# Performance work log

Measured on AMD Instinct MI355X. Metric: run time of the kernel, lower is better.

The kernel has to match this reference:

```python
import jax, jax.numpy as jnp
import numpy as np

L, NH, DH, D, DI, V = 12, 12, 64, 768, 3072, 10000
QLEN, MLEN, CLEN, BSZ = 512, 512, 32, 4
EPS = 1e-5


def _ln(x, g, b):
    m = x.mean(-1, keepdims=True)
    v = ((x - m) ** 2).mean(-1, keepdims=True)
    return (x - m) / jnp.sqrt(v + EPS) * g + b


def _rel_shift(x):
    # x: [B, H, qlen, rlen]; Transformer-XL pad/reshape shift trick
    B, H, q, r = x.shape
    xp = jnp.pad(x, ((0, 0), (0, 0), (0, 0), (1, 0)))
    return xp.reshape(B, H, r + 1, q)[:, :, 1:, :].reshape(B, H, q, r)


def _pos_emb(klen):
    # positions klen-1 .. 0 (relative distances), sinusoidal, dim D
    pos = jnp.arange(klen - 1, -1, -1, dtype=jnp.float32)
    inv = 1.0 / (10000.0 ** (jnp.arange(0, D, 2, dtype=jnp.float32) / D))
    s = pos[:, None] * inv[None, :]
    return jnp.concatenate([jnp.sin(s), jnp.cos(s)], axis=-1)  # [klen, D]


def setup_inputs() -> dict:
    key = jax.random.key(0)
    ks = jax.random.split(key, 21)
    init = lambda k, shape: (0.02 * jax.random.normal(k, shape)).astype(jnp.float32)
    return {
        'x': jax.random.randint(ks[0], (QLEN, BSZ), 0, V),
        'condition': init(ks[1], (CLEN, BSZ, D)) * 50.0,
        'mems': init(ks[2], (L, MLEN, BSZ, D)) * 50.0,
        'emb': init(ks[3], (V, D)),
        'qkv_w': init(ks[4], (L, D, 3 * NH * DH)),
        'r_net_w': init(ks[5], (L, D, NH * DH)),
        'o_w': init(ks[6], (L, NH * DH, D)),
        'ln1_g': jnp.ones((L, D), jnp.float32),
        'ln1_b': jnp.zeros((L, D), jnp.float32),
        'w1': init(ks[7], (L, D, DI)),
        'b1': jnp.zeros((L, DI), jnp.float32),
        'w2': init(ks[8], (L, DI, D)),
        'b2': jnp.zeros((L, D), jnp.float32),
        'ln2_g': jnp.ones((L, D), jnp.float32),
        'ln2_b': jnp.zeros((L, D), jnp.float32),
        'r_w_bias': init(ks[9], (NH, DH)),
        'r_r_bias': init(ks[10], (NH, DH)),
        'proj_w': init(ks[11], (D, V)),
        'proj_b': jnp.zeros((V,), jnp.float32),
    }


def reference(x, condition, mems, emb, qkv_w, r_net_w, o_w, ln1_g, ln1_b,
              w1, b1, w2, b2, ln2_g, ln2_b, r_w_bias, r_r_bias, proj_w, proj_b):
    qlen, bsz = x.shape
    klen = CLEN + MLEN + qlen
    h = emb[x] * jnp.sqrt(jnp.float32(D))  # [qlen, B, D] word emb * sqrt(d_model)
    r = _pos_emb(klen)                      # [klen, D]
    scale = 1.0 / jnp.sqrt(jnp.float32(DH))
    # causal mask: query i may attend to keys j <= CLEN + MLEN + i (True = masked)
    mask = jnp.arange(klen)[None, :] > (jnp.arange(qlen)[:, None] + CLEN + MLEN)
    for l in range(L):
        cat = jnp.concatenate([condition, mems[l], h], axis=0)  # [klen, B, D]
        heads = cat @ qkv_w[l]                                   # [klen, B, 3*NH*DH]
        qh, kh, vh = jnp.split(heads, 3, axis=-1)
        qh = qh[-qlen:].reshape(qlen, bsz, NH, DH)
        kh = kh.reshape(klen, bsz, NH, DH)
        vh = vh.reshape(klen, bsz, NH, DH)
        rk = (r @ r_net_w[l]).reshape(klen, NH, DH)
        AC = jnp.einsum('ibnd,jbnd->bnij', qh + r_w_bias, kh)    # content score
        BD = _rel_shift(jnp.einsum('ibnd,jnd->bnij', qh + r_r_bias, rk))  # position score
        score = (AC + BD) * scale
        score = jnp.where(mask[None, None], -jnp.inf, score)
        prob = jax.nn.softmax(score, axis=-1)
        av = jnp.einsum('bnij,jbnd->ibnd', prob, vh).reshape(qlen, bsz, NH * DH)
        h = _ln(h + av @ o_w[l], ln1_g[l], ln1_b[l])             # post-LN attention
        ff = jax.nn.relu(h @ w1[l] + b1[l]) @ w2[l] + b2[l]
        h = _ln(h + ff, ln2_g[l], ln2_b[l])                      # post-LN FFN
    return h @ proj_w + proj_b  # [qlen, B, n_token] logits
```

## Files before the change

### kernel.cpp

```cpp
#include <hip/hip_runtime.h>
#include <stdint.h>

#define NLAYER 12
#define NH 12
#define DH 64
#define DMODEL 768
#define DI 3072
#define NV 10000
#define QLEN 512
#define MLEN 512
#define CLEN 32
#define BSZ 4
#define KLEN (CLEN + MLEN + QLEN)
#define MQ (QLEN * BSZ)
#define MK (KLEN * BSZ)
#define H3 (3 * NH * DH)
#define HD (NH * DH)
#define NG (BSZ * NH)
#define SROW ((size_t)QLEN * KLEN)
#define KPAD_R 1152
#define NPAD_V 10112

typedef __bf16 bf16;
typedef __bf16 bf16x8 __attribute__((ext_vector_type(8)));
typedef float f32x4 __attribute__((ext_vector_type(4)));

__device__ __forceinline__ void gload16(const void* g, void* l) {
    __builtin_amdgcn_global_load_lds((const __attribute__((address_space(1))) void*)g,
                                     (__attribute__((address_space(3))) void*)l, 16, 0, 0);
}

__device__ __forceinline__ void split_store(float x, bf16* __restrict__ hp,
                                            bf16* __restrict__ lp, size_t off) {
    bf16 h = (bf16)x;
    hp[off] = h;
    lp[off] = (bf16)(x - (float)h);
}

__device__ __forceinline__ void raster(int& bx, int& by) {
    int gx = gridDim.x, gy = gridDim.y;
    int nwg = gx * gy;
    int wgid = blockIdx.y * gx + blockIdx.x;
    int q = nwg >> 3, r = nwg & 7;
    int xcd = wgid & 7, lin = wgid >> 3;
    int swz = (xcd < r ? xcd * (q + 1) : r * (q + 1) + (xcd - r) * q) + lin;
    int gsz = gx * 4;
    int grp = swz / gsz, rem = swz % gsz;
    int rows = gy - grp * 4;
    if (rows > 4) rows = 4;
    bx = rem / rows;
    by = grp * 4 + rem % rows;
}

__global__ __launch_bounds__(256) void k_embed(const int* __restrict__ x,
                                               const float* __restrict__ emb,
                                               float* __restrict__ h) {
    int idx = blockIdx.x * 256 + threadIdx.x;
    if (idx >= MQ * DMODEL) return;
    int row = idx / DMODEL;
    int d = idx % DMODEL;
    int tok = x[row];
    h[idx] = emb[(size_t)tok * DMODEL + d] * 27.712812921102035f;
}

__global__ __launch_bounds__(256) void k_posemb(bf16* __restrict__ rh, bf16* __restrict__ rl) {
    int idx = blockIdx.x * 256 + threadIdx.x;
    if (idx >= KPAD_R * DMODEL) return;
    int k = idx / DMODEL;
    int d = idx % DMODEL;
    float v = 0.0f;
    if (k < KLEN) {
        int pos = KLEN - 1 - k;
        int j = (d < DMODEL / 2) ? d : d - DMODEL / 2;
        double inv = exp(-((double)(2 * j) / (double)DMODEL) * log(10000.0));
        double s = (double)pos * inv;
        v = (d < DMODEL / 2) ? (float)sin(s) : (float)cos(s);
    }
    split_store(v, rh, rl, (size_t)idx);
}

__global__ __launch_bounds__(256) void k_concat(const float* __restrict__ cond,
                                                const float* __restrict__ mem_l,
                                                const float* __restrict__ h,
                                                bf16* __restrict__ catH,
                                                bf16* __restrict__ catL) {
    int idx = blockIdx.x * 256 + threadIdx.x;
    if (idx >= MK * DMODEL) return;
    int row = idx / DMODEL;
    int k = row / BSZ;
    float v;
    if (k < CLEN) v = cond[idx];
    else if (k < CLEN + MLEN) v = mem_l[idx - CLEN * BSZ * DMODEL];
    else v = h[idx - (CLEN + MLEN) * BSZ * DMODEL];
    split_store(v, catH, catL, (size_t)idx);
}

__global__ __launch_bounds__(256) void k_wconv(const float* __restrict__ W,
                                               bf16* __restrict__ Bh,
                                               bf16* __restrict__ Bl,
                                               int K, int N) {
    __shared__ float t[32][33];
    int n0 = blockIdx.x * 32, k0 = blockIdx.y * 32;
    int tc = threadIdx.x & 31, tr = threadIdx.x >> 5;
#pragma unroll
    for (int i = 0; i < 32; i += 8) {
        int n = n0 + tc;
        t[tr + i][tc] = (n < N) ? W[(size_t)(k0 + tr + i) * N + n] : 0.0f;
    }
    __syncthreads();
#pragma unroll
    for (int i = 0; i < 32; i += 8) {
        int n = n0 + tr + i;
        int k = k0 + tc;
        float x = t[tc][tr + i];
        size_t off = (size_t)n * K + k;
        bf16 h = (bf16)x;
        Bh[off] = h;
        Bl[off] = (bf16)(x - (float)h);
    }
}

template <int BM, bool BIAS, bool RELU, bool SPLITOUT>
__global__ __launch_bounds__(256) void k_mgemm(const bf16* __restrict__ Ahi,
                                               const bf16* __restrict__ Alo,
                                               const bf16* __restrict__ Bhi,
                                               const bf16* __restrict__ Blo,
                                               const float* __restrict__ bias,
                                               float* __restrict__ C,
                                               bf16* __restrict__ Chi,
                                               bf16* __restrict__ Clo,
                                               int M, int N, int K, int ldc) {
    constexpr int MI = (BM == 128) ? 4 : 2;
    __shared__ __align__(16) bf16 As[2][BM][32];
    __shared__ __align__(16) bf16 Bs[2][128][32];
    int bx, by;
    raster(bx, by);
    int tid = threadIdx.x;
    int lane = tid & 63;
    int wave = tid >> 6;
    int bm = by * BM, bn = bx * 128;
    int wr = (wave >> 1) * (BM / 2), wc = (wave & 1) * 64;
    int fr = lane & 15;
    int fk = (lane >> 4) * 8;

    const f32x4 fzero = {0.f, 0.f, 0.f, 0.f};
    f32x4 acc[MI][4];
#pragma unroll
    for (int i = 0; i < MI; i++)
#pragma unroll
        for (int j = 0; j < 4; j++) acc[i][j] = fzero;

    int r0 = tid >> 2, p0 = (tid & 3) * 8;
    int r1 = r0 + 64, p1 = p0;

    for (int k0 = 0; k0 < K; k0 += 32) {
        if (BM == 128) {
            gload16(Ahi + (size_t)(bm + r0) * K + k0 + p0, &As[0][r0][p0]);
            gload16(Ahi + (size_t)(bm + r1) * K + k0 + p1, &As[0][r1 & (BM - 1)][p1]);
            gload16(Alo + (size_t)(bm + r0) * K + k0 + p0, &As[1][r0][p0]);
            gload16(Alo + (size_t)(bm + r1) * K + k0 + p1, &As[1][r1 & (BM - 1)][p1]);
        } else {
            gload16(Ahi + (size_t)(bm + r0) * K + k0 + p0, &As[0][r0 & (BM - 1)][p0]);
            gload16(Alo + (size_t)(bm + r0) * K + k0 + p0, &As[1][r0 & (BM - 1)][p0]);
        }
        gload16(Bhi + (size_t)(bn + r0) * K + k0 + p0, &Bs[0][r0][p0]);
        gload16(Bhi + (size_t)(bn + r1) * K + k0 + p1, &Bs[0][r1][p1]);
        gload16(Blo + (size_t)(bn + r0) * K + k0 + p0, &Bs[1][r0][p0]);
        gload16(Blo + (size_t)(bn + r1) * K + k0 + p1, &Bs[1][r1][p1]);
        __syncthreads();

        bf16x8 ah[MI], al[MI], bh[4], bl[4];
#pragma unroll
        for (int mi = 0; mi < MI; mi++) {
            ah[mi] = *(const bf16x8*)&As[0][wr + mi * 16 + fr][fk];
            al[mi] = *(const bf16x8*)&As[1][wr + mi * 16 + fr][fk];
        }
#pragma unroll
        for (int ni = 0; ni < 4; ni++) {
            bh[ni] = *(const bf16x8*)&Bs[0][wc + ni * 16 + fr][fk];
            bl[ni] = *(const bf16x8*)&Bs[1][wc + ni * 16 + fr][fk];
        }
#pragma unroll
        for (int mi = 0; mi < MI; mi++)
#pragma unroll
            for (int ni = 0; ni < 4; ni++) {
                acc[mi][ni] = __builtin_amdgcn_mfma_f32_16x16x32_bf16(ah[mi], bh[ni], acc[mi][ni], 0, 0, 0);
                acc[mi][ni] = __builtin_amdgcn_mfma_f32_16x16x32_bf16(ah[mi], bl[ni], acc[mi][ni], 0, 0, 0);
                acc[mi][ni] = __builtin_amdgcn_mfma_f32_16x16x32_bf16(al[mi], bh[ni], acc[mi][ni], 0, 0, 0);
            }
        __syncthreads();
    }

#pragma unroll
    for (int mi = 0; mi < MI; mi++) {
        int rowb = bm + wr + mi * 16 + (lane >> 4) * 4;
#pragma unroll
        for (int ni = 0; ni < 4; ni++) {
            int col = bn + wc + ni * 16 + fr;
            if (col >= N) continue;
            float bv = BIAS ? bias[col] : 0.0f;
#pragma unroll
            for (int r = 0; r < 4; r++) {
                int row = rowb + r;
                if (row >= M) continue;
                float xv = acc[mi][ni][r] + bv;
                if (RELU) xv = fmaxf(xv, 0.0f);
                size_t off = (size_t)row * ldc + col;
                if (SPLITOUT) {
                    bf16 hh = (bf16)xv;
                    Chi[off] = hh;
                    Clo[off] = (bf16)(xv - (float)hh);
                } else {
                    C[off] = xv;
                }
            }
        }
    }
}

__global__ __launch_bounds__(256) void k_qprep(const float* __restrict__ heads,
                                               const float* __restrict__ rwb,
                                               const float* __restrict__ rrb,
                                               bf16* __restrict__ qwH, bf16* __restrict__ qwL,
                                               bf16* __restrict__ qrH, bf16* __restrict__ qrL) {
    int idx = blockIdx.x * 256 + threadIdx.x;
    if (idx >= NG * QLEN * DH) return;
    int g = idx >> 15;
    int rem = idx & 32767;
    int i = rem >> 6;
    int d = rem & 63;
    int b = g / NH, n = g % NH;
    float q = heads[((size_t)((CLEN + MLEN + i) * BSZ + b)) * H3 + n * DH + d];
    split_store(q + rwb[n * DH + d], qwH, qwL, (size_t)idx);
    split_store(q + rrb[n * DH + d], qrH, qrL, (size_t)idx);
}

__global__ __launch_bounds__(256) void k_kconv(const float* __restrict__ heads,
                                               bf16* __restrict__ khH, bf16* __restrict__ khL,
                                               int g0, int ngc) {
    int idx = blockIdx.x * 256 + threadIdx.x;
    if (idx >= ngc * KPAD_R * DH) return;
    int gl = idx / (KPAD_R * DH);
    int rem = idx % (KPAD_R * DH);
    int j = rem >> 6, d = rem & 63;
    int g = g0 + gl, b = g / NH, n = g % NH;
    float v = (j < KLEN) ? heads[(size_t)(j * BSZ + b) * H3 + HD + n * DH + d] : 0.0f;
    split_store(v, khH, khL, (size_t)idx);
}

__global__ __launch_bounds__(256) void k_vtconv(const float* __restrict__ heads,
                                                bf16* __restrict__ vtH, bf16* __restrict__ vtL,
                                                int g0) {
    __shared__ float t[32][33];
    int gl = blockIdx.z;
    int g = g0 + gl, b = g / NH, n = g % NH;
    int j0 = blockIdx.x * 32, d0 = blockIdx.y * 32;
    int tc = threadIdx.x & 31, tr = threadIdx.x >> 5;
#pragma unroll
    for (int i = 0; i < 32; i += 8)
        t[tr + i][tc] = heads[(size_t)((j0 + tr + i) * BSZ + b) * H3 + 2 * HD + n * DH + d0 + tc];
    __syncthreads();
#pragma unroll
    for (int i = 0; i < 32; i += 8)
        split_store(t[tc][tr + i], vtH, vtL,
                    ((size_t)gl * DH + d0 + tr + i) * KLEN + j0 + tc);
}

template <bool SHIFT>
__global__ __launch_bounds__(256) void k_score(const bf16* __restrict__ QH,
                                               const bf16* __restrict__ QL,
                                               const bf16* __restrict__ KHp,
                                               const bf16* __restrict__ KLp,
                                               float* __restrict__ sAc,
                                               int g0) {
    int gl = blockIdx.z;
    int g = g0 + gl;
    int n = g % NH;
    const bf16* Ah = QH + (size_t)g * QLEN * DH;
    const bf16* Al = QL + (size_t)g * QLEN * DH;
    const bf16 *Bh, *Bl;
    int ldb;
    if (SHIFT) { Bh = KHp + n * DH; Bl = KLp + n * DH; ldb = HD; }
    else { Bh = KHp + (size_t)gl * KPAD_R * DH; Bl = KLp + (size_t)gl * KPAD_R * DH; ldb = DH; }
    float* C = sAc + (size_t)gl * SROW;

    __shared__ __align__(16) bf16 As[2][128][32];
    __shared__ __align__(16) bf16 Bs[2][128][32];
    int tid = threadIdx.x;
    int lane = tid & 63;
    int wave = tid >> 6;
    int bm = blockIdx.y * 128, bn = blockIdx.x * 128;
    int wr = (wave >> 1) * 64, wc = (wave & 1) * 64;
    int fr = lane & 15;
    int fk = (lane >> 4) * 8;

    const f32x4 fzero = {0.f, 0.f, 0.f, 0.f};
    f32x4 acc[4][4];
#pragma unroll
    for (int i = 0; i < 4; i++)
#pragma unroll
        for (int j = 0; j < 4; j++) acc[i][j] = fzero;

    int r0 = tid >> 2, p0 = (tid & 3) * 8;
    int r1 = r0 + 64, p1 = p0;

#pragma unroll
    for (int k0 = 0; k0 < DH; k0 += 32) {
        gload16(Ah + (size_t)(bm + r0) * DH + k0 + p0, &As[0][r0][p0]);
        gload16(Ah + (size_t)(bm + r1) * DH + k0 + p1, &As[0][r1][p1]);
        gload16(Al + (size_t)(bm + r0) * DH + k0 + p0, &As[1][r0][p0]);
        gload16(Al + (size_t)(bm + r1) * DH + k0 + p1, &As[1][r1][p1]);
        gload16(Bh + (size_t)(bn + r0) * ldb + k0 + p0, &Bs[0][r0][p0]);
        gload16(Bh + (size_t)(bn + r1) * ldb + k0 + p1, &Bs[0][r1][p1]);
        gload16(Bl + (size_t)(bn + r0) * ldb + k0 + p0, &Bs[1][r0][p0]);
        gload16(Bl + (size_t)(bn + r1) * ldb + k0 + p1, &Bs[1][r1][p1]);
        __syncthreads();

        bf16x8 ah[4], al[4], bh[4], bl[4];
#pragma unroll
        for (int mi = 0; mi < 4; mi++) {
            ah[mi] = *(const bf16x8*)&As[0][wr + mi * 16 + fr][fk];
            al[mi] = *(const bf16x8*)&As[1][wr + mi * 16 + fr][fk];
        }
#pragma unroll
        for (int ni = 0; ni < 4; ni++) {
            bh[ni] = *(const bf16x8*)&Bs[0][wc + ni * 16 + fr][fk];
            bl[ni] = *(const bf16x8*)&Bs[1][wc + ni * 16 + fr][fk];
        }
#pragma unroll
        for (int mi = 0; mi < 4; mi++)
#pragma unroll
            for (int ni = 0; ni < 4; ni++) {
                acc[mi][ni] = __builtin_amdgcn_mfma_f32_16x16x32_bf16(ah[mi], bh[ni], acc[mi][ni], 0, 0, 0);
                acc[mi][ni] = __builtin_amdgcn_mfma_f32_16x16x32_bf16(ah[mi], bl[ni], acc[mi][ni], 0, 0, 0);
                acc[mi][ni] = __builtin_amdgcn_mfma_f32_16x16x32_bf16(al[mi], bh[ni], acc[mi][ni], 0, 0, 0);
            }
        __syncthreads();
    }

#pragma unroll
    for (int mi = 0; mi < 4; mi++) {
        int rowb = bm + wr + mi * 16 + (lane >> 4) * 4;
#pragma unroll
        for (int ni = 0; ni < 4; ni++) {
            int t = bn + wc + ni * 16 + fr;
            if (t >= KLEN) continue;
#pragma unroll
            for (int r = 0; r < 4; r++) {
                int i = rowb + r;
                if (SHIFT) {
                    int j = t - (QLEN - 1) + i;
                    if (j >= 0) C[(size_t)i * KLEN + j] += acc[mi][ni][r];
                } else {
                    C[(size_t)i * KLEN + t] = acc[mi][ni][r];
                }
            }
        }
    }
}

__global__ __launch_bounds__(256) void k_softmax_p(const float* __restrict__ sAc,
                                                   bf16* __restrict__ P) {
    __shared__ float red[256];
    int i = blockIdx.x;
    int gl = blockIdx.y;
    int tid = threadIdx.x;
    const float* row = sAc + (size_t)gl * SROW + (size_t)i * KLEN;
    bf16* pr = P + (size_t)gl * SROW + (size_t)i * KLEN;
    int len = i + CLEN + MLEN + 1;
    float v[5];
    int cnt = 0;
    float mx = -1e30f;
    for (int j = tid; j < len; j += 256) {
        float s = row[j] * 0.125f;
        v[cnt++] = s;
        mx = fmaxf(mx, s);
    }
    red[tid] = mx;
    __syncthreads();
    for (int st = 128; st > 0; st >>= 1) {
        if (tid < st) red[tid] = fmaxf(red[tid], red[tid + st]);
        __syncthreads();
    }
    float smax = red[0];
    __syncthreads();
    float sum = 0.f;
    cnt = 0;
    for (int j = tid; j < len; j += 256) {
        float e = __expf(v[cnt] - smax);
        v[cnt] = e;
        sum += e;
        cnt++;
    }
    red[tid] = sum;
    __syncthreads();
    for (int st = 128; st > 0; st >>= 1) {
        if (tid < st) red[tid] += red[tid + st];
        __syncthreads();
    }
    float inv = 1.0f / red[0];
    cnt = 0;
    for (int j = tid; j < len; j += 256) pr[j] = (bf16)(v[cnt++] * inv);
    for (int j = tid; j < KLEN; j += 256)
        if (j >= len) pr[j] = (bf16)0.0f;
}

__global__ __launch_bounds__(256) void k_av(const bf16* __restrict__ P,
                                            const bf16* __restrict__ VH,
                                            const bf16* __restrict__ VL,
                                            bf16* __restrict__ atH,
                                            bf16* __restrict__ atL,
                                            int g0) {
    int gl = blockIdx.z;
    int g = g0 + gl;
    int b = g / NH, n = g % NH;
    const bf16* Ap = P + (size_t)gl * SROW;
    const bf16* Vh = VH + (size_t)gl * DH * KLEN;
    const bf16* Vl = VL + (size_t)gl * DH * KLEN;
    __shared__ __align__(16) bf16 As[64][32];
    __shared__ __align__(16) bf16 Bs[2][64][32];
    int tid = threadIdx.x;
    int lane = tid & 63;
    int wave = tid >> 6;
    int bm = blockIdx.y * 64;
    int fr = lane & 15;
    int fk = (lane >> 4) * 8;
    const f32x4 fzero = {0.f, 0.f, 0.f, 0.f};
    f32x4 acc[4] = {fzero, fzero, fzero, fzero};
    int ra = tid >> 2, pa = (tid & 3) * 8;

    for (int k0 = 0; k0 < KLEN; k0 += 32) {
        gload16(Ap + (size_t)(bm + ra) * KLEN + k0 + pa, &As[ra][pa]);
        gload16(Vh + (size_t)ra * KLEN + k0 + pa, &Bs[0][ra][pa]);
        gload16(Vl + (size_t)ra * KLEN + k0 + pa, &Bs[1][ra][pa]);
        __syncthreads();
        bf16x8 a = *(const bf16x8*)&As[wave * 16 + fr][fk];
#pragma unroll
        for (int ni = 0; ni < 4; ni++) {
            bf16x8 bh = *(const bf16x8*)&Bs[0][ni * 16 + fr][fk];
            bf16x8 bl = *(const bf16x8*)&Bs[1][ni * 16 + fr][fk];
            acc[ni] = __builtin_amdgcn_mfma_f32_16x16x32_bf16(a, bh, acc[ni], 0, 0, 0);
            acc[ni] = __builtin_amdgcn_mfma_f32_16x16x32_bf16(a, bl, acc[ni], 0, 0, 0);
        }
        __syncthreads();
    }

#pragma unroll
    for (int ni = 0; ni < 4; ni++) {
        int d = ni * 16 + fr;
#pragma unroll
        for (int r = 0; r < 4; r++) {
            int i = bm + wave * 16 + (lane >> 4) * 4 + r;
            size_t off = (size_t)(i * BSZ + b) * HD + n * DH + d;
            split_store(acc[ni][r], atH, atL, off);
        }
    }
}

__global__ __launch_bounds__(256) void k_add_ln(float* __restrict__ h,
                                                const float* __restrict__ delta,
                                                const float* __restrict__ g,
                                                const float* __restrict__ bta,
                                                bf16* __restrict__ hH,
                                                bf16* __restrict__ hL) {
    __shared__ float xs[DMODEL];
    __shared__ float red[256];
    int row = blockIdx.x;
    int tid = threadIdx.x;
    float* hr = h + (size_t)row * DMODEL;
    const float* dr = delta + (size_t)row * DMODEL;
    float s = 0.f;
    for (int d = tid; d < DMODEL; d += 256) {
        float v = hr[d] + dr[d];
        xs[d] = v;
        s += v;
    }
    red[tid] = s;
    __syncthreads();
    for (int st = 128; st > 0; st >>= 1) {
        if (tid < st) red[tid] += red[tid + st];
        __syncthreads();
    }
    float mean = red[0] * (1.0f / DMODEL);
    __syncthreads();
    float v2 = 0.f;
    for (int d = tid; d < DMODEL; d += 256) {
        float t = xs[d] - mean;
        v2 += t * t;
    }
    red[tid] = v2;
    __syncthreads();
    for (int st = 128; st > 0; st >>= 1) {
        if (tid < st) red[tid] += red[tid + st];
        __syncthreads();
    }
    float inv = rsqrtf(red[0] * (1.0f / DMODEL) + 1e-5f);
    for (int d = tid; d < DMODEL; d += 256) {
        float y = (xs[d] - mean) * inv * g[d] + bta[d];
        hr[d] = y;
        split_store(y, hH, hL, (size_t)row * DMODEL + d);
    }
}

extern "C" void kernel_launch(void* const* d_in, const int* in_sizes, int n_in,
                              void* d_out, int out_size, void* d_ws, size_t ws_size,
                              hipStream_t stream) {
    const int* x = (const int*)d_in[0];
    const float* condition = (const float*)d_in[1];
    const float* mems = (const float*)d_in[2];
    const float* emb = (const float*)d_in[3];
    const float* qkv_w = (const float*)d_in[4];
    const float* r_net_w = (const float*)d_in[5];
    const float* o_w = (const float*)d_in[6];
    const float* ln1_g = (const float*)d_in[7];
    const float* ln1_b = (const float*)d_in[8];
    const float* w1 = (const float*)d_in[9];
    const float* b1 = (const float*)d_in[10];
    const float* w2 = (const float*)d_in[11];
    const float* b2 = (const float*)d_in[12];
    const float* ln2_g = (const float*)d_in[13];
    const float* ln2_b = (const float*)d_in[14];
    const float* r_w_bias = (const float*)d_in[15];
    const float* r_r_bias = (const float*)d_in[16];
    const float* proj_w = (const float*)d_in[17];
    const float* proj_b = (const float*)d_in[18];
    float* out = (float*)d_out;

    float* ws = (float*)d_ws;
    float* h = ws;
    float* heads = h + (size_t)MQ * DMODEL;
    float* delta = heads + (size_t)MK * H3;

    bf16* pb = (bf16*)(delta + (size_t)MQ * DMODEL);
    bf16* rbH = pb; pb += (size_t)KPAD_R * DMODEL;
    bf16* rbL = pb; pb += (size_t)KPAD_R * DMODEL;
    bf16* atH = pb; pb += (size_t)MQ * HD;
    bf16* atL = pb; pb += (size_t)MQ * HD;
    bf16* qwH = pb; pb += (size_t)NG * QLEN * DH;
    bf16* qwL = pb; pb += (size_t)NG * QLEN * DH;
    bf16* qrH = pb; pb += (size_t)NG * QLEN * DH;
    bf16* qrL = pb; pb += (size_t)NG * QLEN * DH;
    bf16* rkH = pb; pb += (size_t)KPAD_R * DMODEL;
    bf16* rkL = pb; pb += (size_t)KPAD_R * DMODEL;

    bf16* R = pb;
    bf16* BtH = R;
    bf16* BtL = BtH + (size_t)NPAD_V * DMODEL;
    bf16* ffnH = BtL + (size_t)NPAD_V * DMODEL;
    bf16* ffnL = ffnH + (size_t)MQ * DI;
    bf16* catH = ffnL + (size_t)MQ * DI;
    bf16* catL = catH + (size_t)MK * DMODEL;
    bf16* hH = catL + (size_t)MK * DMODEL;
    bf16* hL = hH + (size_t)MQ * DMODEL;

    size_t fixed_bytes = (size_t)((char*)R - (char*)d_ws);
    size_t chunk48 = (size_t)48 * (SROW * 6 + KPAD_R * DH * 4 + DH * KLEN * 4);
    int NGC = (ws_size >= fixed_bytes + chunk48) ? 48 : 24;
    float* sAc = (float*)R;
    bf16* Pc = (bf16*)(sAc + (size_t)NGC * SROW);
    bf16* khH = Pc + (size_t)NGC * SROW;
    bf16* khL = khH + (size_t)NGC * KPAD_R * DH;
    bf16* vtH = khL + (size_t)NGC * KPAD_R * DH;
    bf16* vtL = vtH + (size_t)NGC * DH * KLEN;

    dim3 blk(256);
    k_embed<<<dim3((MQ * DMODEL + 255) / 256), blk, 0, stream>>>(x, emb, h);
    k_posemb<<<dim3((KPAD_R * DMODEL + 255) / 256), blk, 0, stream>>>(rbH, rbL);

    for (int l = 0; l < NLAYER; l++) {
        k_concat<<<dim3((MK * DMODEL + 255) / 256), blk, 0, stream>>>(
            condition, mems + (size_t)l * MLEN * BSZ * DMODEL, h, catH, catL);

        k_wconv<<<dim3(H3 / 32, DMODEL / 32), blk, 0, stream>>>(
            qkv_w + (size_t)l * DMODEL * H3, BtH, BtL, DMODEL, H3);
        k_mgemm<128, false, false, false><<<dim3(H3 / 128, MK / 128), blk, 0, stream>>>(
            catH, catL, BtH, BtL, nullptr, heads, nullptr, nullptr, MK, H3, DMODEL, H3);

        k_wconv<<<dim3(HD / 32, DMODEL / 32), blk, 0, stream>>>(
            r_net_w + (size_t)l * DMODEL * HD, BtH, BtL, DMODEL, HD);
        k_mgemm<64, false, false, true><<<dim3(HD / 128, KPAD_R / 64), blk, 0, stream>>>(
            rbH, rbL, BtH, BtL, nullptr, nullptr, rkH, rkL, KPAD_R, HD, DMODEL, HD);

        k_qprep<<<dim3((NG * QLEN * DH + 255) / 256), blk, 0, stream>>>(
            heads, r_w_bias, r_r_bias, qwH, qwL, qrH, qrL);

        for (int g0 = 0; g0 < NG; g0 += NGC) {
            k_kconv<<<dim3((NGC * KPAD_R * DH + 255) / 256), blk, 0, stream>>>(
                heads, khH, khL, g0, NGC);
            k_vtconv<<<dim3(KLEN / 32, DH / 32, NGC), blk, 0, stream>>>(heads, vtH, vtL, g0);
            k_score<false><<<dim3(KPAD_R / 128, QLEN / 128, NGC), blk, 0, stream>>>(
                qwH, qwL, khH, khL, sAc, g0);
            k_score<true><<<dim3(KPAD_R / 128, QLEN / 128, NGC), blk, 0, stream>>>(
                qrH, qrL, rkH, rkL, sAc, g0);
            k_softmax_p<<<dim3(QLEN, NGC), blk, 0, stream>>>(sAc, Pc);
            k_av<<<dim3(1, QLEN / 64, NGC), blk, 0, stream>>>(Pc, vtH, vtL, atH, atL, g0);
        }

        k_wconv<<<dim3(DMODEL / 32, HD / 32), blk, 0, stream>>>(
            o_w + (size_t)l * HD * DMODEL, BtH, BtL, HD, DMODEL);
        k_mgemm<64, false, false, false><<<dim3(DMODEL / 128, MQ / 64), blk, 0, stream>>>(
            atH, atL, BtH, BtL, nullptr, delta, nullptr, nullptr, MQ, DMODEL, HD, DMODEL);

        k_add_ln<<<dim3(MQ), blk, 0, stream>>>(h, delta, ln1_g + (size_t)l * DMODEL,
                                               ln1_b + (size_t)l * DMODEL, hH, hL);

        k_wconv<<<dim3(DI / 32, DMODEL / 32), blk, 0, stream>>>(
            w1 + (size_t)l * DMODEL * DI, BtH, BtL, DMODEL, DI);
        k_mgemm<128, true, true, true><<<dim3(DI / 128, MQ / 128), blk, 0, stream>>>(
            hH, hL, BtH, BtL, b1 + (size_t)l * DI, nullptr, ffnH, ffnL, MQ, DI, DMODEL, DI);

        k_wconv<<<dim3(DMODEL / 32, DI / 32), blk, 0, stream>>>(
            w2 + (size_t)l * DI * DMODEL, BtH, BtL, DI, DMODEL);
        k_mgemm<64, true, false, false><<<dim3(DMODEL / 128, MQ / 64), blk, 0, stream>>>(
            ffnH, ffnL, BtH, BtL, b2 + (size_t)l * DMODEL, delta, nullptr, nullptr,
            MQ, DMODEL, DI, DMODEL);

        k_add_ln<<<dim3(MQ), blk, 0, stream>>>(h, delta, ln2_g + (size_t)l * DMODEL,
                                               ln2_b + (size_t)l * DMODEL, hH, hL);
    }

    k_wconv<<<dim3(NPAD_V / 32, DMODEL / 32), blk, 0, stream>>>(proj_w, BtH, BtL, DMODEL, NV);
    k_mgemm<128, true, false, false><<<dim3(NPAD_V / 128, MQ / 128), blk, 0, stream>>>(
        hH, hL, BtH, BtL, proj_b, out, nullptr, nullptr, MQ, NV, DMODEL, NV);
}
```

Before: 6.495 ms.

## Fuse QKV epilogue into head layouts, skip masked tiles, split-K small GEMMs

The QKV GEMM is split into a K/V kernel and a Q-only kernel that write bf16 hi/lo head-major buffers directly, with the bias add and the 1/8 scale folded in. This removes the fp32 heads buffer and the qprep and kconv kernels. Score tiles that are fully masked and AV k-steps past the causal limit are skipped. The o_w and w2 GEMMs use split-K=2 into two delta buffers that add_ln sums. NGC is fixed at 24, and K padding is zeroed once up front; the tile-skip bounds are hand-derived and risk errors at the edges.

```diff
diff --git a/kernel.cpp b/kernel.cpp
--- a/kernel.cpp
+++ b/kernel.cpp
@@ -20,6 +20,7 @@
 #define SROW ((size_t)QLEN * KLEN)
 #define KPAD_R 1152
 #define NPAD_V 10112
+#define NGC 24
 
 typedef __bf16 bf16;
 typedef __bf16 bf16x8 __attribute__((ext_vector_type(8)));
@@ -77,6 +78,18 @@
         v = (d < DMODEL / 2) ? (float)sin(s) : (float)cos(s);
     }
     split_store(v, rh, rl, (size_t)idx);
+}
+
+__global__ __launch_bounds__(256) void k_zpad(bf16* __restrict__ khH, bf16* __restrict__ khL) {
+    int idx = blockIdx.x * 256 + threadIdx.x;
+    int tot = NG * (KPAD_R - KLEN) * DH;
+    if (idx >= tot) return;
+    int g = idx / ((KPAD_R - KLEN) * DH);
+    int rem = idx % ((KPAD_R - KLEN) * DH);
+    int jr = rem / DH, d = rem % DH;
+    size_t off = ((size_t)g * KPAD_R + KLEN + jr) * DH + d;
+    khH[off] = (bf16)0.0f;
+    khL[off] = (bf16)0.0f;
 }
 
 __global__ __launch_bounds__(256) void k_concat(const float* __restrict__ cond,
@@ -120,7 +133,7 @@
     }
 }
 
-template <int BM, bool BIAS, bool RELU, bool SPLITOUT>
+template <int BM, bool BIAS, bool RELU, bool SPLITOUT, int SK>
 __global__ __launch_bounds__(256) void k_mgemm(const bf16* __restrict__ Ahi,
                                                const bf16* __restrict__ Alo,
                                                const bf16* __restrict__ Bhi,
@@ -135,6 +148,10 @@
     __shared__ __align__(16) bf16 Bs[2][128][32];
     int bx, by;
     raster(bx, by);
+    int z = (SK > 1) ? blockIdx.z : 0;
+    int kb = K / SK;
+    int kbeg = z * kb, kend = kbeg + kb;
+    if (SK > 1) C += (size_t)z * M * ldc;
     int tid = threadIdx.x;
     int lane = tid & 63;
     int wave = tid >> 6;
@@ -153,7 +170,7 @@
     int r0 = tid >> 2, p0 = (tid & 3) * 8;
     int r1 = r0 + 64, p1 = p0;
 
-    for (int k0 = 0; k0 < K; k0 += 32) {
+    for (int k0 = kbeg; k0 < kend; k0 += 32) {
         if (BM == 128) {
             gload16(Ahi + (size_t)(bm + r0) * K + k0 + p0, &As[0][r0][p0]);
             gload16(Ahi + (size_t)(bm + r1) * K + k0 + p1, &As[0][r1 & (BM - 1)][p1]);
@@ -198,7 +215,7 @@
         for (int ni = 0; ni < 4; ni++) {
             int col = bn + wc + ni * 16 + fr;
             if (col >= N) continue;
-            float bv = BIAS ? bias[col] : 0.0f;
+            float bv = (BIAS && z == 0) ? bias[col] : 0.0f;
 #pragma unroll
             for (int r = 0; r < 4; r++) {
                 int row = rowb + r;
@@ -218,52 +235,130 @@
     }
 }
 
-__global__ __launch_bounds__(256) void k_qprep(const float* __restrict__ heads,
-                                               const float* __restrict__ rwb,
-                                               const float* __restrict__ rrb,
-                                               bf16* __restrict__ qwH, bf16* __restrict__ qwL,
-                                               bf16* __restrict__ qrH, bf16* __restrict__ qrL) {
-    int idx = blockIdx.x * 256 + threadIdx.x;
-    if (idx >= NG * QLEN * DH) return;
-    int g = idx >> 15;
-    int rem = idx & 32767;
-    int i = rem >> 6;
-    int d = rem & 63;
-    int b = g / NH, n = g % NH;
-    float q = heads[((size_t)((CLEN + MLEN + i) * BSZ + b)) * H3 + n * DH + d];
-    split_store(q + rwb[n * DH + d], qwH, qwL, (size_t)idx);
-    split_store(q + rrb[n * DH + d], qrH, qrL, (size_t)idx);
-}
-
-__global__ __launch_bounds__(256) void k_kconv(const float* __restrict__ heads,
-                                               bf16* __restrict__ khH, bf16* __restrict__ khL,
-                                               int g0, int ngc) {
-    int idx = blockIdx.x * 256 + threadIdx.x;
-    if (idx >= ngc * KPAD_R * DH) return;
-    int gl = idx / (KPAD_R * DH);
-    int rem = idx % (KPAD_R * DH);
-    int j = rem >> 6, d = rem & 63;
-    int g = g0 + gl, b = g / NH, n = g % NH;
-    float v = (j < KLEN) ? heads[(size_t)(j * BSZ + b) * H3 + HD + n * DH + d] : 0.0f;
-    split_store(v, khH, khL, (size_t)idx);
-}
-
-__global__ __launch_bounds__(256) void k_vtconv(const float* __restrict__ heads,
-                                                bf16* __restrict__ vtH, bf16* __restrict__ vtL,
-                                                int g0) {
-    __shared__ float t[32][33];
+template <int MODE>
+__global__ __launch_bounds__(256) void k_mgemm_qkv(const bf16* __restrict__ Ahi,
+                                                   const bf16* __restrict__ Alo,
+                                                   const bf16* __restrict__ Bhi,
+                                                   const bf16* __restrict__ Blo,
+                                                   const float* __restrict__ rwb,
+                                                   const float* __restrict__ rrb,
+                                                   bf16* __restrict__ P0H, bf16* __restrict__ P0L,
+                                                   bf16* __restrict__ P1H, bf16* __restrict__ P1L) {
+    constexpr int K = DMODEL;
+    __shared__ __align__(16) bf16 As[2][128][32];
+    __shared__ __align__(16) bf16 Bs[2][128][32];
+    int bx, by;
+    raster(bx, by);
+    int tid = threadIdx.x;
+    int lane = tid & 63;
+    int wave = tid >> 6;
+    int bm = by * 128, bn = bx * 128;
+    int wr = (wave >> 1) * 64, wc = (wave & 1) * 64;
+    int fr = lane & 15;
+    int fk = (lane >> 4) * 8;
+
+    const f32x4 fzero = {0.f, 0.f, 0.f, 0.f};
+    f32x4 acc[4][4];
+#pragma unroll
+    for (int i = 0; i < 4; i++)
+#pragma unroll
+        for (int j = 0; j < 4; j++) acc[i][j] = fzero;
+
+    int r0 = tid >> 2, p0 = (tid & 3) * 8;
+    int r1 = r0 + 64, p1 = p0;
+
+    for (int k0 = 0; k0 < K; k0 += 32) {
+        gload16(Ahi + (size_t)(bm + r0) * K + k0 + p0, &As[0][r0][p0]);
+        gload16(Ahi + (size_t)(bm + r1) * K + k0 + p1, &As[0][r1][p1]);
+        gload16(Alo + (size_t)(bm + r0) * K + k0 + p0, &As[1][r0][p0]);
+        gload16(Alo + (size_t)(bm + r1) * K + k0 + p1, &As[1][r1][p1]);
+        gload16(Bhi + (size_t)(bn + r0) * K + k0 + p0, &Bs[0][r0][p0]);
+        gload16(Bhi + (size_t)(bn + r1) * K + k0 + p1, &Bs[0][r1][p1]);
+        gload16(Blo + (size_t)(bn + r0) * K + k0 + p0, &Bs[1][r0][p0]);
+        gload16(Blo + (size_t)(bn + r1) * K + k0 + p1, &Bs[1][r1][p1]);
+        __syncthreads();
+
+        bf16x8 ah[4], al[4], bh[4], bl[4];
+#pragma unroll
+        for (int mi = 0; mi < 4; mi++) {
+            ah[mi] = *(const bf16x8*)&As[0][wr + mi * 16 + fr][fk];
+            al[mi] = *(const bf16x8*)&As[1][wr + mi * 16 + fr][fk];
+        }
+#pragma unroll
+        for (int ni = 0; ni < 4; ni++) {
+            bh[ni] = *(const bf16x8*)&Bs[0][wc + ni * 16 + fr][fk];
+            bl[ni] = *(const bf16x8*)&Bs[1][wc + ni * 16 + fr][fk];
+        }
+#pragma unroll
+        for (int mi = 0; mi < 4; mi++)
+#pragma unroll
+            for (int ni = 0; ni < 4; ni++) {
+                acc[mi][ni] = __builtin_amdgcn_mfma_f32_16x16x32_bf16(ah[mi], bh[ni], acc[mi][ni], 0, 0, 0);
+                acc[mi][ni] = __builtin_amdgcn_mfma_f32_16x16x32_bf16(ah[mi], bl[ni], acc[mi][ni], 0, 0, 0);
+                acc[mi][ni] = __builtin_amdgcn_mfma_f32_16x16x32_bf16(al[mi], bh[ni], acc[mi][ni], 0, 0, 0);
+            }
+        __syncthreads();
+    }
+
+#pragma unroll
+    for (int mi = 0; mi < 4; mi++) {
+        int rowb = bm + wr + mi * 16 + (lane >> 4) * 4;
+#pragma unroll
+        for (int ni = 0; ni < 4; ni++) {
+            int col = bn + wc + ni * 16 + fr;
+#pragma unroll
+            for (int r = 0; r < 4; r++) {
+                int row = rowb + r;
+                float xv = acc[mi][ni][r];
+                int b = row & 3;
+                if (MODE == 0) {
+                    int i = row >> 2;
+                    int g = b * NH + (col >> 6);
+                    int d = col & 63;
+                    size_t off = ((size_t)g * QLEN + i) * DH + d;
+                    split_store((xv + rwb[col]) * 0.125f, P0H, P0L, off);
+                    split_store((xv + rrb[col]) * 0.125f, P1H, P1L, off);
+                } else {
+                    int j = row >> 2;
+                    if (col < HD) {
+                        int g = b * NH + (col >> 6);
+                        int d = col & 63;
+                        split_store(xv, P0H, P0L, ((size_t)g * KPAD_R + j) * DH + d);
+                    } else {
+                        int c2 = col - HD;
+                        int g = b * NH + (c2 >> 6);
+                        int d = c2 & 63;
+                        split_store(xv, P1H, P1L, ((size_t)g * KLEN + j) * DH + d);
+                    }
+                }
+            }
+        }
+    }
+}
+
+__global__ __launch_bounds__(256) void k_vtconv_b(const bf16* __restrict__ vH,
+                                                  const bf16* __restrict__ vL,
+                                                  bf16* __restrict__ vtH,
+                                                  bf16* __restrict__ vtL,
+                                                  int g0) {
+    __shared__ bf16 th[32][33], tl[32][33];
     int gl = blockIdx.z;
-    int g = g0 + gl, b = g / NH, n = g % NH;
+    int g = g0 + gl;
     int j0 = blockIdx.x * 32, d0 = blockIdx.y * 32;
     int tc = threadIdx.x & 31, tr = threadIdx.x >> 5;
 #pragma unroll
-    for (int i = 0; i < 32; i += 8)
-        t[tr + i][tc] = heads[(size_t)((j0 + tr + i) * BSZ + b) * H3 + 2 * HD + n * DH + d0 + tc];
+    for (int i = 0; i < 32; i += 8) {
+        size_t src = ((size_t)g * KLEN + j0 + tr + i) * DH + d0 + tc;
+        th[tr + i][tc] = vH[src];
+        tl[tr + i][tc] = vL[src];
+    }
     __syncthreads();
 #pragma unroll
-    for (int i = 0; i < 32; i += 8)
-        split_store(t[tc][tr + i], vtH, vtL,
-                    ((size_t)gl * DH + d0 + tr + i) * KLEN + j0 + tc);
+    for (int i = 0; i < 32; i += 8) {
+        size_t dst = ((size_t)gl * DH + d0 + tr + i) * KLEN + j0 + tc;
+        vtH[dst] = th[tc][tr + i];
+        vtL[dst] = tl[tc][tr + i];
+    }
 }
 
 template <bool SHIFT>
@@ -273,6 +368,9 @@
                                                const bf16* __restrict__ KLp,
                                                float* __restrict__ sAc,
                                                int g0) {
+    int bm = blockIdx.y * 128, bn = blockIdx.x * 128;
+    if (!SHIFT && bn >= bm + 672) return;
+    if (SHIFT && bn + bm < 257) return;
     int gl = blockIdx.z;
     int g = g0 + gl;
     int n = g % NH;
@@ -281,7 +379,7 @@
     const bf16 *Bh, *Bl;
     int ldb;
     if (SHIFT) { Bh = KHp + n * DH; Bl = KLp + n * DH; ldb = HD; }
-    else { Bh = KHp + (size_t)gl * KPAD_R * DH; Bl = KLp + (size_t)gl * KPAD_R * DH; ldb = DH; }
+    else { Bh = KHp + (size_t)g * KPAD_R * DH; Bl = KLp + (size_t)g * KPAD_R * DH; ldb = DH; }
     float* C = sAc + (size_t)gl * SROW;
 
     __shared__ __align__(16) bf16 As[2][128][32];
@@ -289,7 +387,6 @@
     int tid = threadIdx.x;
     int lane = tid & 63;
     int wave = tid >> 6;
-    int bm = blockIdx.y * 128, bn = blockIdx.x * 128;
     int wr = (wave >> 1) * 64, wc = (wave & 1) * 64;
     int fr = lane & 15;
     int fk = (lane >> 4) * 8;
@@ -372,7 +469,7 @@
     int cnt = 0;
     float mx = -1e30f;
     for (int j = tid; j < len; j += 256) {
-        float s = row[j] * 0.125f;
+        float s = row[j];
         v[cnt++] = s;
         mx = fmaxf(mx, s);
     }
@@ -428,8 +525,10 @@
     const f32x4 fzero = {0.f, 0.f, 0.f, 0.f};
     f32x4 acc[4] = {fzero, fzero, fzero, fzero};
     int ra = tid >> 2, pa = (tid & 3) * 8;
-
-    for (int k0 = 0; k0 < KLEN; k0 += 32) {
+    int kmax = bm + 608;
+    if (kmax > KLEN) kmax = KLEN;
+
+    for (int k0 = 0; k0 < kmax; k0 += 32) {
         gload16(Ap + (size_t)(bm + ra) * KLEN + k0 + pa, &As[ra][pa]);
         gload16(Vh + (size_t)ra * KLEN + k0 + pa, &Bs[0][ra][pa]);
         gload16(Vl + (size_t)ra * KLEN + k0 + pa, &Bs[1][ra][pa]);
@@ -458,7 +557,8 @@
 }
 
 __global__ __launch_bounds__(256) void k_add_ln(float* __restrict__ h,
-                                                const float* __restrict__ delta,
+                                                const float* __restrict__ d0,
+                                                const float* __restrict__ d1,
                                                 const float* __restrict__ g,
                                                 const float* __restrict__ bta,
                                                 bf16* __restrict__ hH,
@@ -468,10 +568,11 @@
     int row = blockIdx.x;
     int tid = threadIdx.x;
     float* hr = h + (size_t)row * DMODEL;
-    const float* dr = delta + (size_t)row * DMODEL;
+    const float* dr0 = d0 + (size_t)row * DMODEL;
+    const float* dr1 = d1 + (size_t)row * DMODEL;
     float s = 0.f;
     for (int d = tid; d < DMODEL; d += 256) {
-        float v = hr[d] + dr[d];
+        float v = hr[d] + dr0[d] + dr1[d];
         xs[d] = v;
         s += v;
     }
@@ -528,20 +629,24 @@
 
     float* ws = (float*)d_ws;
     float* h = ws;
-    float* heads = h + (size_t)MQ * DMODEL;
-    float* delta = heads + (size_t)MK * H3;
-
-    bf16* pb = (bf16*)(delta + (size_t)MQ * DMODEL);
+    float* delta = h + (size_t)MQ * DMODEL;
+    float* delta2 = delta + (size_t)MQ * DMODEL;
+
+    bf16* pb = (bf16*)(delta2 + (size_t)MQ * DMODEL);
     bf16* rbH = pb; pb += (size_t)KPAD_R * DMODEL;
     bf16* rbL = pb; pb += (size_t)KPAD_R * DMODEL;
+    bf16* rkH = pb; pb += (size_t)KPAD_R * DMODEL;
+    bf16* rkL = pb; pb += (size_t)KPAD_R * DMODEL;
     bf16* atH = pb; pb += (size_t)MQ * HD;
     bf16* atL = pb; pb += (size_t)MQ * HD;
     bf16* qwH = pb; pb += (size_t)NG * QLEN * DH;
     bf16* qwL = pb; pb += (size_t)NG * QLEN * DH;
     bf16* qrH = pb; pb += (size_t)NG * QLEN * DH;
     bf16* qrL = pb; pb += (size_t)NG * QLEN * DH;
-    bf16* rkH = pb; pb += (size_t)KPAD_R * DMODEL;
-    bf16* rkL = pb; pb += (size_t)KPAD_R * DMODEL;
+    bf16* khH = pb; pb += (size_t)NG * KPAD_R * DH;
+    bf16* khL = pb; pb += (size_t)NG * KPAD_R * DH;
+    bf16* vH_ = pb; pb += (size_t)NG * KLEN * DH;
+    bf16* vL_ = pb; pb += (size_t)NG * KLEN * DH;
 
     bf16* R = pb;
     bf16* BtH = R;
@@ -553,19 +658,15 @@
     bf16* hH = catL + (size_t)MK * DMODEL;
     bf16* hL = hH + (size_t)MQ * DMODEL;
 
-    size_t fixed_bytes = (size_t)((char*)R - (char*)d_ws);
-    size_t chunk48 = (size_t)48 * (SROW * 6 + KPAD_R * DH * 4 + DH * KLEN * 4);
-    int NGC = (ws_size >= fixed_bytes + chunk48) ? 48 : 24;
     float* sAc = (float*)R;
     bf16* Pc = (bf16*)(sAc + (size_t)NGC * SROW);
-    bf16* khH = Pc + (size_t)NGC * SROW;
-    bf16* khL = khH + (size_t)NGC * KPAD_R * DH;
-    bf16* vtH = khL + (size_t)NGC * KPAD_R * DH;
+    bf16* vtH = Pc + (size_t)NGC * SROW;
     bf16* vtL = vtH + (size_t)NGC * DH * KLEN;
 
     dim3 blk(256);
     k_embed<<<dim3((MQ * DMODEL + 255) / 256), blk, 0, stream>>>(x, emb, h);
     k_posemb<<<dim3((KPAD_R * DMODEL + 255) / 256), blk, 0, stream>>>(rbH, rbL);
+    k_zpad<<<dim3((NG * (KPAD_R - KLEN) * DH + 255) / 256), blk, 0, stream>>>(khH, khL);
 
     for (int l = 0; l < NLAYER; l++) {
         k_concat<<<dim3((MK * DMODEL + 255) / 256), blk, 0, stream>>>(
@@ -573,21 +674,20 @@
 
         k_wconv<<<dim3(H3 / 32, DMODEL / 32), blk, 0, stream>>>(
             qkv_w + (size_t)l * DMODEL * H3, BtH, BtL, DMODEL, H3);
-        k_mgemm<128, false, false, false><<<dim3(H3 / 128, MK / 128), blk, 0, stream>>>(
-            catH, catL, BtH, BtL, nullptr, heads, nullptr, nullptr, MK, H3, DMODEL, H3);
+        k_mgemm_qkv<1><<<dim3((2 * HD) / 128, MK / 128), blk, 0, stream>>>(
+            catH, catL, BtH + (size_t)HD * DMODEL, BtL + (size_t)HD * DMODEL,
+            nullptr, nullptr, khH, khL, vH_, vL_);
+        k_mgemm_qkv<0><<<dim3(HD / 128, MQ / 128), blk, 0, stream>>>(
+            catH + (size_t)(CLEN + MLEN) * BSZ * DMODEL, catL + (size_t)(CLEN + MLEN) * BSZ * DMODEL,
+            BtH, BtL, r_w_bias, r_r_bias, qwH, qwL, qrH, qrL);
 
         k_wconv<<<dim3(HD / 32, DMODEL / 32), blk, 0, stream>>>(
             r_net_w + (size_t)l * DMODEL * HD, BtH, BtL, DMODEL, HD);
-        k_mgemm<64, false, false, true><<<dim3(HD / 128, KPAD_R / 64), blk, 0, stream>>>(
+        k_mgemm<64, false, false, true, 1><<<dim3(HD / 128, KPAD_R / 64), blk, 0, stream>>>(
             rbH, rbL, BtH, BtL, nullptr, nullptr, rkH, rkL, KPAD_R, HD, DMODEL, HD);
 
-        k_qprep<<<dim3((NG * QLEN * DH + 255) / 256), blk, 0, stream>>>(
-            heads, r_w_bias, r_r_bias, qwH, qwL, qrH, qrL);
-
         for (int g0 = 0; g0 < NG; g0 += NGC) {
-            k_kconv<<<dim3((NGC * KPAD_R * DH + 255) / 256), blk, 0, stream>>>(
-                heads, khH, khL, g0, NGC);
-            k_vtconv<<<dim3(KLEN / 32, DH / 32, NGC), blk, 0, stream>>>(heads, vtH, vtL, g0);
+            k_vtconv_b<<<dim3(KLEN / 32, DH / 32, NGC), blk, 0, stream>>>(vH_, vL_, vtH, vtL, g0);
             k_score<false><<<dim3(KPAD_R / 128, QLEN / 128, NGC), blk, 0, stream>>>(
                 qwH, qwL, khH, khL, sAc, g0);
             k_score<true><<<dim3(KPAD_R / 128, QLEN / 128, NGC), blk, 0, stream>>>(
@@ -598,28 +698,28 @@
 
         k_wconv<<<dim3(DMODEL / 32, HD / 32), blk, 0, stream>>>(
             o_w + (size_t)l * HD * DMODEL, BtH, BtL, HD, DMODEL);
-        k_mgemm<64, false, false, false><<<dim3(DMODEL / 128, MQ / 64), blk, 0, stream>>>(
+        k_mgemm<64, false, false, false, 2><<<dim3(DMODEL / 128, MQ / 64, 2), blk, 0, stream>>>(
             atH, atL, BtH, BtL, nullptr, delta, nullptr, nullptr, MQ, DMODEL, HD, DMODEL);
 
-        k_add_ln<<<dim3(MQ), blk, 0, stream>>>(h, delta, ln1_g + (size_t)l * DMODEL,
+        k_add_ln<<<dim3(MQ), blk, 0, stream>>>(h, delta, delta2, ln1_g + (size_t)l * DMODEL,
                                                ln1_b + (size_t)l * DMODEL, hH, hL);
 
         k_wconv<<<dim3(DI / 32, DMODEL / 32), blk, 0, stream>>>(
             w1 + (size_t)l * DMODEL * DI, BtH, BtL, DMODEL, DI);
-        k_mgemm<128, true, true, true><<<dim3(DI / 128, MQ / 128), blk, 0, stream>>>(
+        k_mgemm<128, true, true, true, 1><<<dim3(DI / 128, MQ / 128), blk, 0, stream>>>(
             hH, hL, BtH, BtL, b1 + (size_t)l * DI, nullptr, ffnH, ffnL, MQ, DI, DMODEL, DI);
 
         k_wconv<<<dim3(DMODEL / 32, DI / 32), blk, 0, stream>>>(
             w2 + (size_t)l * DI * DMODEL, BtH, BtL, DI, DMODEL);
-        k_mgemm<64, true, false, false><<<dim3(DMODEL / 128, MQ / 64), blk, 0, stream>>>(
+        k_mgemm<64, true, false, false, 2><<<dim3(DMODEL / 128, MQ / 64, 2), blk, 0, stream>>>(
             ffnH, ffnL, BtH, BtL, b2 + (size_t)l * DMODEL, delta, nullptr, nullptr,
             MQ, DMODEL, DI, DMODEL);
 
-        k_add_ln<<<dim3(MQ), blk, 0, stream>>>(h, delta, ln2_g + (size_t)l * DMODEL,
+        k_add_ln<<<dim3(MQ), blk, 0, stream>>>(h, delta, delta2, ln2_g + (size_t)l * DMODEL,
                                                ln2_b + (size_t)l * DMODEL, hH, hL);
     }
 
     k_wconv<<<dim3(NPAD_V / 32, DMODEL / 32), blk, 0, stream>>>(proj_w, BtH, BtL, DMODEL, NV);
-    k_mgemm<128, true, false, false><<<dim3(NPAD_V / 128, MQ / 128), blk, 0, stream>>>(
+    k_mgemm<128, true, false, false, 1><<<dim3(NPAD_V / 128, MQ / 128), blk, 0, stream>>>(
         hH, hL, BtH, BtL, proj_b, out, nullptr, nullptr, MQ, NV, DMODEL, NV);
 }
```

Result: no change. 6.509 ms (+0.2%).
